# Performance work log

Measured on AMD Instinct MI355X. Metric: run time of the kernel, lower is better.

Reference implementation:

```python
import jax, jax.numpy as jnp
import numpy as np

N, C, H, W = 8, 80, 100, 152          # batch, fg classes, stride-8 feature map of 800x1216 image
STRIDE = 8
P = H * W                              # points in this level
PRE_NMS_THRESH = 0.05                  # cfg.post.INFERENCE_TH
PRE_NMS_TOP_N = 1000                   # cfg.post.PRE_NMS_TOP_N
NMS_THRESH = 0.6                       # cfg.post.NMS_TH
POST_NMS_TOP_N = 100                   # cfg.post.DETECTIONS_PER_IMG
MIN_SIZE = 0.0
CLASS_OFFSET = 1.0e5                   # per-class NMS via coordinate-offset trick


def setup_inputs():
    key = jax.random.key(0)
    k1, k2, k3 = jax.random.split(key, 3)
    ys, xs = jnp.meshgrid(jnp.arange(H), jnp.arange(W), indexing='ij')
    locations = (jnp.stack([xs.reshape(-1), ys.reshape(-1)], axis=1).astype(jnp.float32) * STRIDE + STRIDE // 2)
    box_cls = jax.random.normal(k1, (N, C, H, W), jnp.float32) - 2.0
    box_regression = jax.random.uniform(k2, (N, 4, H, W), jnp.float32) * 64.0
    centerness = jax.random.normal(k3, (N, 1, H, W), jnp.float32)
    im_info = jnp.tile(jnp.array([[H * STRIDE, W * STRIDE]], jnp.float32), (N, 1))
    return {'locations': locations, 'box_cls': box_cls, 'box_regression': box_regression,
            'centerness': centerness, 'im_info': im_info}


def _iou_matrix(boxes):
    # boxes: [K, 4] (x1, y1, x2, y2)
    area = jnp.clip(boxes[:, 2] - boxes[:, 0], 0) * jnp.clip(boxes[:, 3] - boxes[:, 1], 0)
    lt = jnp.maximum(boxes[:, None, :2], boxes[None, :, :2])
    rb = jnp.minimum(boxes[:, None, 2:], boxes[None, :, 2:])
    wh = jnp.clip(rb - lt, 0)
    inter = wh[..., 0] * wh[..., 1]
    return inter / (area[:, None] + area[None, :] - inter + 1e-9)


def _single_image(locations, cls_logits, reg, ctr_logits, info):
    # [C,H,W] -> [P,C] matches permute(0,2,3,1).reshape(-1,C)
    cls = jax.nn.sigmoid(cls_logits.reshape(C, P).T)
    ctr = jax.nn.sigmoid(ctr_logits.reshape(P))
    cand = cls > PRE_NMS_THRESH
    scores = cls * ctr[:, None]
    flat = jnp.where(cand, scores, 0.0).reshape(-1)          # [P*C], zeros = non-candidates
    topv, topi = jax.lax.top_k(flat, PRE_NMS_TOP_N)          # pre-NMS top-n (sorted desc)
    loc = topi // C
    label = topi % C + 1
    valid = topv > 0.0
    r = reg.reshape(4, P).T[loc]                             # [K, 4] (l, t, r, b)
    pt = locations[loc]                                      # [K, 2]
    h_im, w_im = info[0], info[1]
    x1 = jnp.clip(pt[:, 0] - r[:, 0], 0.0, w_im - 1.0)
    y1 = jnp.clip(pt[:, 1] - r[:, 1], 0.0, h_im - 1.0)
    x2 = jnp.clip(pt[:, 0] + r[:, 2], 0.0, w_im - 1.0)
    y2 = jnp.clip(pt[:, 1] + r[:, 3], 0.0, h_im - 1.0)
    boxes = jnp.stack([x1, y1, x2, y2], axis=1)
    valid = valid & (x2 - x1 >= MIN_SIZE) & (y2 - y1 >= MIN_SIZE)  # remove_small_boxes
    sc = jnp.where(valid, topv, 0.0)
    # offset boxes by class so cross-class IoU is 0 -> equivalent to per-class NMS
    ob = boxes + (label.astype(boxes.dtype) * CLASS_OFFSET)[:, None]
    iou = _iou_matrix(ob)
    idx = jnp.arange(PRE_NMS_TOP_N)
    def body(i, keep):
        alive = keep[i] & valid[i]
        sup = alive & (iou[i] > NMS_THRESH) & (idx > i)
        return keep & ~sup
    keep = jax.lax.fori_loop(0, PRE_NMS_TOP_N, body, valid)  # greedy NMS (score-sorted)
    final_sc = jnp.where(keep, sc, 0.0)
    fv, fi = jax.lax.top_k(final_sc, POST_NMS_TOP_N)         # detections-per-image cap
    out = jnp.concatenate([boxes[fi], label[fi][:, None].astype(boxes.dtype), fv[:, None]], axis=1)
    return jnp.where((fv > 0.0)[:, None], out, 0.0)          # [POST_NMS_TOP_N, 6]


def reference(locations, box_cls, box_regression, centerness, im_info):
    # -> [N, POST_NMS_TOP_N, 6] = (x1, y1, x2, y2, label, score), zero-padded rows invalid
    return jax.vmap(lambda c, r, t, i: _single_image(locations, c, r, t, i))(
        box_cls, box_regression, centerness, im_info)
```

## Files before the change

### kernel.cpp

```cpp
#include <hip/hip_runtime.h>
#include <stdint.h>

#define NIMG 8
#define NCLS 80
#define HF 100
#define WF 152
#define NPTS (HF*WF)
#define NPC (NPTS*NCLS)
#define NF4 (NPC/4)
#define TOPK 1000
#define NSH 8
#define SHCAP 512
#define SORTN 4096
#define LBUF 1024
#define POSTK 100
#define HBLK 297
#define RBLK (SORTN/256)
#define SCHUNK 32
#define SSTRIDE 9500
#define SM_T 65

static constexpr size_t B_CNT  = 0;
static constexpr size_t B_META = B_CNT + (size_t)NIMG*NSH*4;
static constexpr size_t B_SKEY = (B_META + NIMG*4*4 + 7) & ~(size_t)7;
static constexpr size_t B_CTRS = (B_SKEY + (size_t)NIMG*1024*8 + 15) & ~(size_t)15;
static constexpr size_t B_CAND = (B_CTRS + (size_t)NIMG*NPTS*4 + 15) & ~(size_t)15;
static constexpr size_t B_BOX  = B_CAND + (size_t)NIMG*NSH*SHCAP*8;
static constexpr size_t B_OBOX = B_BOX + (size_t)NIMG*TOPK*16;
static constexpr size_t B_SC   = B_OBOX + (size_t)NIMG*TOPK*16;
static constexpr size_t B_VAL  = B_SC + (size_t)NIMG*TOPK*4;
static constexpr size_t B_LAB  = B_VAL + (size_t)NIMG*TOPK*4;
static constexpr size_t B_KEEP = B_LAB + (size_t)NIMG*TOPK*4;
#define ZWORDS (NIMG*NSH + NIMG*4)

__device__ __forceinline__ float sigm(float x){ return 1.0f / (1.0f + expf(-x)); }

__global__ void __launch_bounds__(256)
k_ctrsig(const float* __restrict__ ctr, float* __restrict__ ctr_sig,
         uint32_t* __restrict__ zr, uint64_t* __restrict__ skey){
  const int gid = blockIdx.x * 256 + threadIdx.x;
  const int nthr = 119 * 256;
  if (gid < NIMG*NPTS/4){
    float4 v = ((const float4*)ctr)[gid];
    float4 o;
    o.x = sigm(v.x); o.y = sigm(v.y); o.z = sigm(v.z); o.w = sigm(v.w);
    ((float4*)ctr_sig)[gid] = o;
  }
  for (int i = gid; i < ZWORDS; i += nthr) zr[i] = 0u;
  for (int i = gid; i < NIMG*1024; i += nthr) skey[i] = 0ull;
}

__global__ void __launch_bounds__(256)
k_sample(const float* __restrict__ box_cls, const float* __restrict__ ctr_sig,
         uint32_t* __restrict__ meta){
  __shared__ uint32_t h[4096];
  __shared__ uint32_t psum[256], suff[256];
  const int n = blockIdx.x;
  const int t = threadIdx.x;
  for (int i = t; i < 4096; i += 256) h[i] = 0;
  __syncthreads();
  const float4* cls4 = (const float4*)(box_cls + (size_t)n * NPC);
  const float* cs = ctr_sig + (size_t)n * NPTS;
  for (int c0 = 0; c0 < SCHUNK; c0 += 4){
    float4 a[4], b[4];
    #pragma unroll
    for (int k = 0; k < 4; ++k){
      int g = (c0 + k) * SSTRIDE + t;
      a[k] = cls4[g];
      uint32_t p0 = ((uint32_t)(g << 2)) % (uint32_t)NPTS;
      b[k] = *(const float4*)(cs + p0);
    }
    __builtin_amdgcn_sched_barrier(0);
    #pragma unroll
    for (int k = 0; k < 4; ++k){
      float sv[4] = {a[k].x, a[k].y, a[k].z, a[k].w};
      float cv[4] = {b[k].x, b[k].y, b[k].z, b[k].w};
      #pragma unroll
      for (int j = 0; j < 4; ++j){
        float s = sigm(sv[j]);
        if (s > 0.05f){
          float sc = s * cv[j];
          if (sc > 0.0f) atomicAdd(&h[__float_as_uint(sc) >> 18], 1u);
        }
      }
    }
  }
  __syncthreads();
  uint32_t s = 0;
  #pragma unroll
  for (int i = 0; i < 16; ++i) s += h[t * 16 + i];
  psum[t] = s;
  __syncthreads();
  if (t == 0){
    uint32_t acc = 0;
    for (int seg = 255; seg >= 0; --seg){ suff[seg] = acc; acc += psum[seg]; }
  }
  __syncthreads();
  if (suff[t] < SM_T && suff[t] + psum[t] >= SM_T){
    uint32_t acc = suff[t];
    for (int b = t * 16 + 15; b >= t * 16; --b){
      uint32_t hb = h[b];
      if (acc + hb >= SM_T){
        meta[n * 4 + 1] = ((uint32_t)b) << 18;
        break;
      }
      acc += hb;
    }
  }
}

__global__ void __launch_bounds__(256)
k_main(const float* __restrict__ box_cls, const float* __restrict__ ctr_sig,
       const uint32_t* __restrict__ meta,
       uint32_t* __restrict__ cnt, uint64_t* __restrict__ cand){
  __shared__ uint64_t buf[LBUF];
  __shared__ uint32_t lcnt;
  __shared__ uint32_t gbase;
  const int n = blockIdx.y;
  const uint32_t Traw = meta[n * 4 + 1];
  if (threadIdx.x == 0) lcnt = 0;
  __syncthreads();
  const float4* cls4 = (const float4*)(box_cls + (size_t)n * NPC);
  const float* cs = ctr_sig + (size_t)n * NPTS;
  const int base4 = blockIdx.x * 1024 + threadIdx.x;
  float4 a[4], b[4];
  int p0a[4], ca[4];
  bool ok[4];
  #pragma unroll
  for (int k = 0; k < 4; ++k){
    int i4 = base4 + k * 256;
    ok[k] = (i4 < NF4);
    if (ok[k]){
      a[k] = cls4[i4];
      uint32_t e0 = (uint32_t)(i4 << 2);
      uint32_t c = e0 / (uint32_t)NPTS;
      uint32_t p0 = e0 - c * (uint32_t)NPTS;
      ca[k] = (int)c; p0a[k] = (int)p0;
      b[k] = *(const float4*)(cs + p0);
    }
  }
  __builtin_amdgcn_sched_barrier(0);
  #pragma unroll
  for (int k = 0; k < 4; ++k){
    if (!ok[k]) continue;
    float sv[4] = {a[k].x, a[k].y, a[k].z, a[k].w};
    float cv[4] = {b[k].x, b[k].y, b[k].z, b[k].w};
    #pragma unroll
    for (int j = 0; j < 4; ++j){
      float s = sigm(sv[j]);
      if (s > 0.05f){
        float sc = s * cv[j];
        if (sc > 0.0f){
          uint32_t bits = __float_as_uint(sc);
          if (bits >= Traw){
            uint32_t f = (uint32_t)(p0a[k] + j) * NCLS + (uint32_t)ca[k];
            uint32_t pos = atomicAdd(&lcnt, 1u);
            if (pos < LBUF)
              buf[pos] = ((uint64_t)bits << 32) | (uint64_t)(0xFFFFFFFFu - f);
          }
        }
      }
    }
  }
  __syncthreads();
  uint32_t c = lcnt; if (c > LBUF) c = LBUF;
  const int sh = blockIdx.x & (NSH - 1);
  if (threadIdx.x == 0 && c) gbase = atomicAdd(&cnt[n * NSH + sh], c);
  __syncthreads();
  for (uint32_t i = threadIdx.x; i < c; i += 256){
    uint32_t p = gbase + i;
    if (p < SHCAP) cand[(((size_t)n * NSH + sh) << 9) + p] = buf[i];
  }
}

__global__ void __launch_bounds__(1024)
k_fallback(const float* __restrict__ box_cls, const float* __restrict__ ctr_sig,
           const uint32_t* __restrict__ meta,
           uint32_t* __restrict__ cnt, uint64_t* __restrict__ cand){
  __shared__ uint32_t h[4096];
  __shared__ uint32_t psum[256], suff[256];
  __shared__ uint32_t ok_s, T14_s, ctr_s;
  const int n = blockIdx.x;
  const int t = threadIdx.x;
  if (t == 0){
    uint32_t total = 0, bad = 0;
    for (int s = 0; s < NSH; ++s){
      uint32_t c = cnt[n * NSH + s];
      total += c; bad |= (c > SHCAP) ? 1u : 0u;
    }
    uint32_t Traw = meta[n * 4 + 1];
    ok_s = (!bad && (total >= TOPK || Traw == 0u)) ? 1u : 0u;
    T14_s = 0; ctr_s = 0;
  }
  __syncthreads();
  if (ok_s) return;
  for (int i = t; i < 4096; i += 1024) h[i] = 0;
  __syncthreads();
  const float* cls = box_cls + (size_t)n * NPC;
  const float* cs = ctr_sig + (size_t)n * NPTS;
  for (int e = t; e < NPC; e += 1024){
    int c = e / NPTS, p = e - c * NPTS;
    float s = sigm(cls[e]);
    if (s > 0.05f){
      float sc = s * cs[p];
      if (sc > 0.0f) atomicAdd(&h[__float_as_uint(sc) >> 18], 1u);
    }
  }
  __syncthreads();
  if (t < 256){
    uint32_t s = 0;
    #pragma unroll
    for (int i = 0; i < 16; ++i) s += h[t * 16 + i];
    psum[t] = s;
  }
  __syncthreads();
  if (t == 0){
    uint32_t acc = 0;
    for (int seg = 255; seg >= 0; --seg){ suff[seg] = acc; acc += psum[seg]; }
  }
  __syncthreads();
  if (t < 256 && suff[t] < TOPK && suff[t] + psum[t] >= TOPK){
    uint32_t acc = suff[t];
    for (int b = t * 16 + 15; b >= t * 16; --b){
      uint32_t hb = h[b];
      if (acc + hb >= TOPK){ T14_s = (uint32_t)b; break; }
      acc += hb;
    }
  }
  __syncthreads();
  const uint32_t Traw2 = T14_s << 18;
  if (t < NSH) cnt[n * NSH + t] = 0;
  __syncthreads();
  for (int e = t; e < NPC; e += 1024){
    int c = e / NPTS, p = e - c * NPTS;
    float s = sigm(cls[e]);
    if (s > 0.05f){
      float sc = s * cs[p];
      if (sc > 0.0f){
        uint32_t bits = __float_as_uint(sc);
        if (bits >= Traw2){
          uint32_t f = (uint32_t)p * NCLS + (uint32_t)c;
          uint32_t pos = atomicAdd(&ctr_s, 1u);
          if (pos < SORTN)
            cand[((size_t)n * NSH << 9) + pos] = ((uint64_t)bits << 32) | (uint64_t)(0xFFFFFFFFu - f);
        }
      }
    }
  }
  __syncthreads();
  if (t < NSH){
    uint32_t total = ctr_s; if (total > SORTN) total = SORTN;
    int lo = t * SHCAP;
    cnt[n * NSH + t] = ((int)total > lo) ? ((total - lo > SHCAP) ? SHCAP : total - lo) : 0u;
  }
}

__global__ void __launch_bounds__(256)
k_rank(const uint32_t* __restrict__ cnt, const uint64_t* __restrict__ cand,
       uint64_t* __restrict__ skey){
  __shared__ alignas(16) uint64_t keys[SORTN + 64];
  __shared__ uint32_t cs_s[NSH], pre_s[NSH + 1];
  const int n = blockIdx.y;
  const int t = threadIdx.x;
  const int lane = t & 63;
  if (t == 0){
    uint32_t acc = 0;
    for (int s = 0; s < NSH; ++s){
      uint32_t c = cnt[n * NSH + s]; if (c > SHCAP) c = SHCAP;
      cs_s[s] = c; pre_s[s] = acc; acc += c;
    }
    pre_s[NSH] = acc;
  }
  __syncthreads();
  const int total = (int)pre_s[NSH];
  const int base = blockIdx.x * 256;
  if (base >= total) return;
  for (int i = t; i < SORTN; i += 256){
    int s = i >> 9, j = i & (SHCAP - 1);
    if ((uint32_t)j < cs_s[s])
      keys[pre_s[s] + j] = cand[(((size_t)n * NSH + s) << 9) + j];
  }
  if (t < 64) keys[total + t] = 0ull;
  __syncthreads();
  const int g = base + t;
  const uint64_t my = (g < total) ? keys[g] : 0ull;
  uint32_t rank = 0;
  const int tot64 = (total + 63) & ~63;
  for (int i = 0; i < tot64; i += 64){
    uint64_t kv = keys[i + lane];
    uint32_t kvlo = (uint32_t)kv, kvhi = (uint32_t)(kv >> 32);
    #pragma unroll
    for (int s = 0; s < 64; ++s){
      uint32_t ohi = (uint32_t)__builtin_amdgcn_readlane((int)kvhi, s);
      uint32_t olo = (uint32_t)__builtin_amdgcn_readlane((int)kvlo, s);
      uint64_t other = ((uint64_t)ohi << 32) | (uint64_t)olo;
      rank += (other > my) ? 1u : 0u;
    }
  }
  if (g < total && rank < TOPK)
    skey[(size_t)n * 1024 + rank] = my;
}

__global__ void __launch_bounds__(1024)
k_decode(const uint64_t* __restrict__ skey,
         const float* __restrict__ locations, const float* __restrict__ box_reg,
         const float* __restrict__ im_info,
         float* __restrict__ boxw, float* __restrict__ oboxw, float* __restrict__ scw,
         uint32_t* __restrict__ valw, uint32_t* __restrict__ labw){
  const int n = blockIdx.x;
  const int t = threadIdx.x;
  if (t < TOPK){
    uint64_t kk = skey[(size_t)n * 1024 + t];
    uint32_t bits = (uint32_t)(kk >> 32);
    uint32_t fi = 0xFFFFFFFFu - (uint32_t)(kk & 0xFFFFFFFFull);
    float v = __uint_as_float(bits);
    int loc = 0, ci = 0;
    if (v > 0.0f){ loc = (int)(fi / NCLS); ci = (int)(fi - (uint32_t)loc * NCLS); }
    float px = locations[2 * loc], py = locations[2 * loc + 1];
    const float* rg = box_reg + (size_t)n * 4 * NPTS;
    float rl = rg[loc], rt = rg[NPTS + loc], rr = rg[2 * NPTS + loc], rb = rg[3 * NPTS + loc];
    float h_im = im_info[n * 2 + 0], w_im = im_info[n * 2 + 1];
    float x1 = fminf(fmaxf(px - rl, 0.0f), w_im - 1.0f);
    float y1 = fminf(fmaxf(py - rt, 0.0f), h_im - 1.0f);
    float x2 = fminf(fmaxf(px + rr, 0.0f), w_im - 1.0f);
    float y2 = fminf(fmaxf(py + rb, 0.0f), h_im - 1.0f);
    bool valid = (v > 0.0f) && (__fsub_rn(x2, x1) >= 0.0f) && (__fsub_rn(y2, y1) >= 0.0f);
    float scv = valid ? v : 0.0f;
    float lab = (float)(ci + 1);
    float off = __fmul_rn(lab, 100000.0f);
    size_t b4 = ((size_t)n * TOPK + t) * 4;
    boxw[b4 + 0] = x1; boxw[b4 + 1] = y1; boxw[b4 + 2] = x2; boxw[b4 + 3] = y2;
    oboxw[b4 + 0] = __fadd_rn(x1, off); oboxw[b4 + 1] = __fadd_rn(y1, off);
    oboxw[b4 + 2] = __fadd_rn(x2, off); oboxw[b4 + 3] = __fadd_rn(y2, off);
    size_t b1 = (size_t)n * TOPK + t;
    scw[b1] = scv; valw[b1] = valid ? 1u : 0u; labw[b1] = (uint32_t)(ci + 1);
  }
}

__global__ void __launch_bounds__(64)
k_nms(const uint32_t* __restrict__ labw, const float* __restrict__ oboxw,
      const uint32_t* __restrict__ valw, uint32_t* __restrict__ keepw){
  const int n = blockIdx.y;
  const int c = blockIdx.x;
  const int L = threadIdx.x;
  __shared__ uint16_t lst_s[TOPK];
  const uint32_t target = (uint32_t)(c + 1);
  uint32_t kcnt = 0;
  for (int i0 = 0; i0 < TOPK; i0 += 64){
    int slot = i0 + L;
    uint32_t lab = (slot < TOPK) ? labw[n * TOPK + slot] : 0u;
    bool m = (lab == target);
    uint64_t mask = __ballot(m);
    uint32_t pre = (uint32_t)__popcll(mask & ((1ull << L) - 1ull));
    if (m) lst_s[kcnt + pre] = (uint16_t)slot;
    kcnt += (uint32_t)__popcll(mask);
  }
  __syncthreads();
  if (kcnt == 0) return;
  if (kcnt <= 64){
    int gi = 0, kp = 0;
    float b0 = 0, b1 = 0, b2 = 0, b3 = 0, ar = 0;
    if (L < (int)kcnt){
      gi = (int)lst_s[L];
      size_t a4 = ((size_t)n * TOPK + gi) * 4;
      b0 = oboxw[a4 + 0]; b1 = oboxw[a4 + 1]; b2 = oboxw[a4 + 2]; b3 = oboxw[a4 + 3];
      kp = (valw[n * TOPK + gi] != 0) ? 1 : 0;
      ar = __fmul_rn(fmaxf(__fsub_rn(b2, b0), 0.0f), fmaxf(__fsub_rn(b3, b1), 0.0f));
    }
    for (int i = 0; i + 1 < (int)kcnt; ++i){
      int alive = __shfl(kp, i);
      float xi0 = __shfl(b0, i), xi1 = __shfl(b1, i), xi2 = __shfl(b2, i), xi3 = __shfl(b3, i);
      float ai = __shfl(ar, i);
      if (alive && L > i && kp){
        float ltx = fmaxf(xi0, b0), lty = fmaxf(xi1, b1);
        float rbx = fminf(xi2, b2), rby = fminf(xi3, b3);
        float w = fmaxf(__fsub_rn(rbx, ltx), 0.0f);
        float h = fmaxf(__fsub_rn(rby, lty), 0.0f);
        float inter = __fmul_rn(w, h);
        float den = __fadd_rn(__fsub_rn(__fadd_rn(ai, ar), inter), 1e-9f);
        if (inter / den > 0.6f) kp = 0;
      }
    }
    if (L < (int)kcnt) keepw[n * TOPK + gi] = (uint32_t)kp;
  } else if (L == 0){
    for (uint32_t i = 0; i < kcnt; ++i){
      int gi = (int)lst_s[i];
      keepw[n * TOPK + gi] = valw[n * TOPK + gi];
    }
    for (uint32_t i = 0; i < kcnt; ++i){
      int gi = (int)lst_s[i];
      if (!keepw[n * TOPK + gi]) continue;
      size_t a4 = ((size_t)n * TOPK + gi) * 4;
      float x0 = oboxw[a4], x1 = oboxw[a4 + 1], x2 = oboxw[a4 + 2], x3 = oboxw[a4 + 3];
      float ai = __fmul_rn(fmaxf(__fsub_rn(x2, x0), 0.0f), fmaxf(__fsub_rn(x3, x1), 0.0f));
      for (uint32_t j = i + 1; j < kcnt; ++j){
        int gj = (int)lst_s[j];
        if (!keepw[n * TOPK + gj]) continue;
        size_t c4 = ((size_t)n * TOPK + gj) * 4;
        float y0 = oboxw[c4], y1 = oboxw[c4 + 1], y2 = oboxw[c4 + 2], y3 = oboxw[c4 + 3];
        float aj = __fmul_rn(fmaxf(__fsub_rn(y2, y0), 0.0f), fmaxf(__fsub_rn(y3, y1), 0.0f));
        float ltx = fmaxf(x0, y0), lty = fmaxf(x1, y1);
        float rbx = fminf(x2, y2), rby = fminf(x3, y3);
        float w = fmaxf(__fsub_rn(rbx, ltx), 0.0f);
        float h = fmaxf(__fsub_rn(rby, lty), 0.0f);
        float inter = __fmul_rn(w, h);
        float den = __fadd_rn(__fsub_rn(__fadd_rn(ai, aj), inter), 1e-9f);
        if (inter / den > 0.6f) keepw[n * TOPK + gj] = 0;
      }
    }
  }
}

__global__ void __launch_bounds__(256)
k_final(const uint32_t* __restrict__ keepw, const float* __restrict__ boxw,
        const uint32_t* __restrict__ labw, const float* __restrict__ scw,
        float* __restrict__ out){
  const int n = blockIdx.x;
  __shared__ uint16_t fi_s[TOPK];
  __shared__ uint32_t wsum[4];
  const int t = threadIdx.x;
  const int i0 = t * 4;
  uint32_t f[4];
  #pragma unroll
  for (int j = 0; j < 4; ++j)
    f[j] = (i0 + j < TOPK) ? keepw[n * TOPK + i0 + j] : 0u;
  uint32_t lsum = f[0] + f[1] + f[2] + f[3];
  uint32_t sc = lsum;
  #pragma unroll
  for (int d = 1; d < 64; d <<= 1){
    uint32_t v = __shfl_up(sc, d);
    if ((t & 63) >= d) sc += v;
  }
  if ((t & 63) == 63) wsum[t >> 6] = sc;
  __syncthreads();
  uint32_t base = sc - lsum;
  for (int w = 0; w < (t >> 6); ++w) base += wsum[w];
  uint32_t p = base;
  #pragma unroll
  for (int j = 0; j < 4; ++j){
    if (f[j]){ if (p < TOPK) fi_s[p] = (uint16_t)(i0 + j); ++p; }
  }
  __syncthreads();
  uint32_t total = wsum[0] + wsum[1] + wsum[2] + wsum[3];
  if (t < POSTK){
    float* row = out + ((size_t)n * POSTK + t) * 6;
    if (t < (int)total){
      int i = (int)fi_s[t];
      size_t b4 = ((size_t)n * TOPK + i) * 4;
      row[0] = boxw[b4]; row[1] = boxw[b4 + 1]; row[2] = boxw[b4 + 2]; row[3] = boxw[b4 + 3];
      row[4] = (float)labw[n * TOPK + i]; row[5] = scw[n * TOPK + i];
    } else {
      row[0] = 0.0f; row[1] = 0.0f; row[2] = 0.0f;
      row[3] = 0.0f; row[4] = 0.0f; row[5] = 0.0f;
    }
  }
}

extern "C" void kernel_launch(void* const* d_in, const int* in_sizes, int n_in,
                              void* d_out, int out_size, void* d_ws, size_t ws_size,
                              hipStream_t stream){
  const float* locations = (const float*)d_in[0];
  const float* box_cls   = (const float*)d_in[1];
  const float* box_reg   = (const float*)d_in[2];
  const float* ctr       = (const float*)d_in[3];
  const float* im_info   = (const float*)d_in[4];
  float* out = (float*)d_out;
  char* ws = (char*)d_ws;
  uint32_t* cnt  = (uint32_t*)(ws + B_CNT);
  uint32_t* meta = (uint32_t*)(ws + B_META);
  uint64_t* skey = (uint64_t*)(ws + B_SKEY);
  float*    ctrs = (float*)(ws + B_CTRS);
  uint64_t* cand = (uint64_t*)(ws + B_CAND);
  float*    boxw  = (float*)(ws + B_BOX);
  float*    oboxw = (float*)(ws + B_OBOX);
  float*    scw   = (float*)(ws + B_SC);
  uint32_t* valw  = (uint32_t*)(ws + B_VAL);
  uint32_t* labw  = (uint32_t*)(ws + B_LAB);
  uint32_t* keepw = (uint32_t*)(ws + B_KEEP);

  k_ctrsig<<<dim3(119), 256, 0, stream>>>(ctr, ctrs, cnt, skey);
  k_sample<<<dim3(NIMG), 256, 0, stream>>>(box_cls, ctrs, meta);
  k_main<<<dim3(HBLK, NIMG), 256, 0, stream>>>(box_cls, ctrs, meta, cnt, cand);
  k_fallback<<<dim3(NIMG), 1024, 0, stream>>>(box_cls, ctrs, meta, cnt, cand);
  k_rank<<<dim3(RBLK, NIMG), 256, 0, stream>>>(cnt, cand, skey);
  k_decode<<<NIMG, 1024, 0, stream>>>(skey, locations, box_reg, im_info,
                                      boxw, oboxw, scw, valw, labw);
  k_nms<<<dim3(NCLS, NIMG), 64, 0, stream>>>(labw, oboxw, valw, keepw);
  k_final<<<NIMG, 256, 0, stream>>>(keepw, boxw, labw, scw, out);
}
```

Baseline: 185.1 us.

## Merge prep kernels and fuse NMS with final gather via last-block counter

Merges the centerness-sigmoid/zeroing kernel and the threshold-sampling kernel into one launch. The sampling blocks now compute the centerness sigmoid inline from raw input instead of reading the precomputed buffer. NMS and the final compaction are fused: each per-class block bumps a per-image done counter, and the last block compacts the keep flags and writes the output rows. This removes two launches and their gaps, at the cost of atomics, fences and redundant sigmoid work in the sampler.

```diff
diff --git a/kernel.cpp b/kernel.cpp
--- a/kernel.cpp
+++ b/kernel.cpp
@@ -19,9 +19,11 @@
 #define SCHUNK 32
 #define SSTRIDE 9500
 #define SM_T 65
+#define PBLK 127
 
 static constexpr size_t B_CNT  = 0;
-static constexpr size_t B_META = B_CNT + (size_t)NIMG*NSH*4;
+static constexpr size_t B_DONE = B_CNT + (size_t)NIMG*NSH*4;
+static constexpr size_t B_META = B_DONE + NIMG*4;
 static constexpr size_t B_SKEY = (B_META + NIMG*4*4 + 7) & ~(size_t)7;
 static constexpr size_t B_CTRS = (B_SKEY + (size_t)NIMG*1024*8 + 15) & ~(size_t)15;
 static constexpr size_t B_CAND = (B_CTRS + (size_t)NIMG*NPTS*4 + 15) & ~(size_t)15;
@@ -31,50 +33,51 @@
 static constexpr size_t B_VAL  = B_SC + (size_t)NIMG*TOPK*4;
 static constexpr size_t B_LAB  = B_VAL + (size_t)NIMG*TOPK*4;
 static constexpr size_t B_KEEP = B_LAB + (size_t)NIMG*TOPK*4;
-#define ZWORDS (NIMG*NSH + NIMG*4)
+#define ZWORDS (NIMG*NSH + NIMG)
 
 __device__ __forceinline__ float sigm(float x){ return 1.0f / (1.0f + expf(-x)); }
 
 __global__ void __launch_bounds__(256)
-k_ctrsig(const float* __restrict__ ctr, float* __restrict__ ctr_sig,
-         uint32_t* __restrict__ zr, uint64_t* __restrict__ skey){
-  const int gid = blockIdx.x * 256 + threadIdx.x;
-  const int nthr = 119 * 256;
-  if (gid < NIMG*NPTS/4){
-    float4 v = ((const float4*)ctr)[gid];
-    float4 o;
-    o.x = sigm(v.x); o.y = sigm(v.y); o.z = sigm(v.z); o.w = sigm(v.w);
-    ((float4*)ctr_sig)[gid] = o;
-  }
-  for (int i = gid; i < ZWORDS; i += nthr) zr[i] = 0u;
-  for (int i = gid; i < NIMG*1024; i += nthr) skey[i] = 0ull;
-}
-
-__global__ void __launch_bounds__(256)
-k_sample(const float* __restrict__ box_cls, const float* __restrict__ ctr_sig,
-         uint32_t* __restrict__ meta){
+k_prep(const float* __restrict__ ctr, const float* __restrict__ box_cls,
+       float* __restrict__ ctr_sig, uint32_t* __restrict__ zr,
+       uint64_t* __restrict__ skey, uint32_t* __restrict__ meta){
+  const int b = blockIdx.x;
+  const int t = threadIdx.x;
+  if (b < 119){
+    const int gid = b * 256 + t;
+    const int nthr = 119 * 256;
+    if (gid < NIMG*NPTS/4){
+      float4 v = ((const float4*)ctr)[gid];
+      float4 o;
+      o.x = sigm(v.x); o.y = sigm(v.y); o.z = sigm(v.z); o.w = sigm(v.w);
+      ((float4*)ctr_sig)[gid] = o;
+    }
+    for (int i = gid; i < ZWORDS; i += nthr) zr[i] = 0u;
+    for (int i = gid; i < NIMG*1024; i += nthr) skey[i] = 0ull;
+    return;
+  }
+  const int n = b - 119;
   __shared__ uint32_t h[4096];
   __shared__ uint32_t psum[256], suff[256];
-  const int n = blockIdx.x;
-  const int t = threadIdx.x;
   for (int i = t; i < 4096; i += 256) h[i] = 0;
+  if (t == 0) meta[n * 4 + 1] = 0u;
   __syncthreads();
   const float4* cls4 = (const float4*)(box_cls + (size_t)n * NPC);
-  const float* cs = ctr_sig + (size_t)n * NPTS;
+  const float* ctq = ctr + (size_t)n * NPTS;
   for (int c0 = 0; c0 < SCHUNK; c0 += 4){
-    float4 a[4], b[4];
+    float4 a[4], rb[4];
     #pragma unroll
     for (int k = 0; k < 4; ++k){
       int g = (c0 + k) * SSTRIDE + t;
       a[k] = cls4[g];
       uint32_t p0 = ((uint32_t)(g << 2)) % (uint32_t)NPTS;
-      b[k] = *(const float4*)(cs + p0);
+      rb[k] = *(const float4*)(ctq + p0);
     }
     __builtin_amdgcn_sched_barrier(0);
     #pragma unroll
     for (int k = 0; k < 4; ++k){
       float sv[4] = {a[k].x, a[k].y, a[k].z, a[k].w};
-      float cv[4] = {b[k].x, b[k].y, b[k].z, b[k].w};
+      float cv[4] = {sigm(rb[k].x), sigm(rb[k].y), sigm(rb[k].z), sigm(rb[k].w)};
       #pragma unroll
       for (int j = 0; j < 4; ++j){
         float s = sigm(sv[j]);
@@ -98,10 +101,10 @@
   __syncthreads();
   if (suff[t] < SM_T && suff[t] + psum[t] >= SM_T){
     uint32_t acc = suff[t];
-    for (int b = t * 16 + 15; b >= t * 16; --b){
-      uint32_t hb = h[b];
+    for (int bb = t * 16 + 15; bb >= t * 16; --bb){
+      uint32_t hb = h[bb];
       if (acc + hb >= SM_T){
-        meta[n * 4 + 1] = ((uint32_t)b) << 18;
+        meta[n * 4 + 1] = ((uint32_t)bb) << 18;
         break;
       }
       acc += hb;
@@ -338,8 +341,11 @@
 }
 
 __global__ void __launch_bounds__(64)
-k_nms(const uint32_t* __restrict__ labw, const float* __restrict__ oboxw,
-      const uint32_t* __restrict__ valw, uint32_t* __restrict__ keepw){
+k_nmsfinal(const uint32_t* __restrict__ labw, const float* __restrict__ oboxw,
+           const uint32_t* __restrict__ valw, const float* __restrict__ boxw,
+           const float* __restrict__ scw,
+           uint32_t* __restrict__ keepw, uint32_t* __restrict__ done,
+           float* __restrict__ out){
   const int n = blockIdx.y;
   const int c = blockIdx.x;
   const int L = threadIdx.x;
@@ -356,102 +362,91 @@
     kcnt += (uint32_t)__popcll(mask);
   }
   __syncthreads();
-  if (kcnt == 0) return;
-  if (kcnt <= 64){
-    int gi = 0, kp = 0;
-    float b0 = 0, b1 = 0, b2 = 0, b3 = 0, ar = 0;
-    if (L < (int)kcnt){
-      gi = (int)lst_s[L];
-      size_t a4 = ((size_t)n * TOPK + gi) * 4;
-      b0 = oboxw[a4 + 0]; b1 = oboxw[a4 + 1]; b2 = oboxw[a4 + 2]; b3 = oboxw[a4 + 3];
-      kp = (valw[n * TOPK + gi] != 0) ? 1 : 0;
-      ar = __fmul_rn(fmaxf(__fsub_rn(b2, b0), 0.0f), fmaxf(__fsub_rn(b3, b1), 0.0f));
-    }
-    for (int i = 0; i + 1 < (int)kcnt; ++i){
-      int alive = __shfl(kp, i);
-      float xi0 = __shfl(b0, i), xi1 = __shfl(b1, i), xi2 = __shfl(b2, i), xi3 = __shfl(b3, i);
-      float ai = __shfl(ar, i);
-      if (alive && L > i && kp){
-        float ltx = fmaxf(xi0, b0), lty = fmaxf(xi1, b1);
-        float rbx = fminf(xi2, b2), rby = fminf(xi3, b3);
-        float w = fmaxf(__fsub_rn(rbx, ltx), 0.0f);
-        float h = fmaxf(__fsub_rn(rby, lty), 0.0f);
-        float inter = __fmul_rn(w, h);
-        float den = __fadd_rn(__fsub_rn(__fadd_rn(ai, ar), inter), 1e-9f);
-        if (inter / den > 0.6f) kp = 0;
-      }
-    }
-    if (L < (int)kcnt) keepw[n * TOPK + gi] = (uint32_t)kp;
-  } else if (L == 0){
-    for (uint32_t i = 0; i < kcnt; ++i){
-      int gi = (int)lst_s[i];
-      keepw[n * TOPK + gi] = valw[n * TOPK + gi];
-    }
-    for (uint32_t i = 0; i < kcnt; ++i){
-      int gi = (int)lst_s[i];
-      if (!keepw[n * TOPK + gi]) continue;
-      size_t a4 = ((size_t)n * TOPK + gi) * 4;
-      float x0 = oboxw[a4], x1 = oboxw[a4 + 1], x2 = oboxw[a4 + 2], x3 = oboxw[a4 + 3];
-      float ai = __fmul_rn(fmaxf(__fsub_rn(x2, x0), 0.0f), fmaxf(__fsub_rn(x3, x1), 0.0f));
-      for (uint32_t j = i + 1; j < kcnt; ++j){
-        int gj = (int)lst_s[j];
-        if (!keepw[n * TOPK + gj]) continue;
-        size_t c4 = ((size_t)n * TOPK + gj) * 4;
-        float y0 = oboxw[c4], y1 = oboxw[c4 + 1], y2 = oboxw[c4 + 2], y3 = oboxw[c4 + 3];
-        float aj = __fmul_rn(fmaxf(__fsub_rn(y2, y0), 0.0f), fmaxf(__fsub_rn(y3, y1), 0.0f));
-        float ltx = fmaxf(x0, y0), lty = fmaxf(x1, y1);
-        float rbx = fminf(x2, y2), rby = fminf(x3, y3);
-        float w = fmaxf(__fsub_rn(rbx, ltx), 0.0f);
-        float h = fmaxf(__fsub_rn(rby, lty), 0.0f);
-        float inter = __fmul_rn(w, h);
-        float den = __fadd_rn(__fsub_rn(__fadd_rn(ai, aj), inter), 1e-9f);
-        if (inter / den > 0.6f) keepw[n * TOPK + gj] = 0;
-      }
-    }
-  }
-}
-
-__global__ void __launch_bounds__(256)
-k_final(const uint32_t* __restrict__ keepw, const float* __restrict__ boxw,
-        const uint32_t* __restrict__ labw, const float* __restrict__ scw,
-        float* __restrict__ out){
-  const int n = blockIdx.x;
-  __shared__ uint16_t fi_s[TOPK];
-  __shared__ uint32_t wsum[4];
-  const int t = threadIdx.x;
-  const int i0 = t * 4;
-  uint32_t f[4];
-  #pragma unroll
-  for (int j = 0; j < 4; ++j)
-    f[j] = (i0 + j < TOPK) ? keepw[n * TOPK + i0 + j] : 0u;
-  uint32_t lsum = f[0] + f[1] + f[2] + f[3];
-  uint32_t sc = lsum;
-  #pragma unroll
-  for (int d = 1; d < 64; d <<= 1){
-    uint32_t v = __shfl_up(sc, d);
-    if ((t & 63) >= d) sc += v;
-  }
-  if ((t & 63) == 63) wsum[t >> 6] = sc;
-  __syncthreads();
-  uint32_t base = sc - lsum;
-  for (int w = 0; w < (t >> 6); ++w) base += wsum[w];
-  uint32_t p = base;
-  #pragma unroll
-  for (int j = 0; j < 4; ++j){
-    if (f[j]){ if (p < TOPK) fi_s[p] = (uint16_t)(i0 + j); ++p; }
-  }
-  __syncthreads();
-  uint32_t total = wsum[0] + wsum[1] + wsum[2] + wsum[3];
-  if (t < POSTK){
-    float* row = out + ((size_t)n * POSTK + t) * 6;
-    if (t < (int)total){
-      int i = (int)fi_s[t];
-      size_t b4 = ((size_t)n * TOPK + i) * 4;
-      row[0] = boxw[b4]; row[1] = boxw[b4 + 1]; row[2] = boxw[b4 + 2]; row[3] = boxw[b4 + 3];
-      row[4] = (float)labw[n * TOPK + i]; row[5] = scw[n * TOPK + i];
-    } else {
-      row[0] = 0.0f; row[1] = 0.0f; row[2] = 0.0f;
-      row[3] = 0.0f; row[4] = 0.0f; row[5] = 0.0f;
+  if (kcnt != 0){
+    if (kcnt <= 64){
+      int gi = 0, kp = 0;
+      float b0 = 0, b1 = 0, b2 = 0, b3 = 0, ar = 0;
+      if (L < (int)kcnt){
+        gi = (int)lst_s[L];
+        size_t a4 = ((size_t)n * TOPK + gi) * 4;
+        b0 = oboxw[a4 + 0]; b1 = oboxw[a4 + 1]; b2 = oboxw[a4 + 2]; b3 = oboxw[a4 + 3];
+        kp = (valw[n * TOPK + gi] != 0) ? 1 : 0;
+        ar = __fmul_rn(fmaxf(__fsub_rn(b2, b0), 0.0f), fmaxf(__fsub_rn(b3, b1), 0.0f));
+      }
+      for (int i = 0; i + 1 < (int)kcnt; ++i){
+        int alive = __shfl(kp, i);
+        float xi0 = __shfl(b0, i), xi1 = __shfl(b1, i), xi2 = __shfl(b2, i), xi3 = __shfl(b3, i);
+        float ai = __shfl(ar, i);
+        if (alive && L > i && kp){
+          float ltx = fmaxf(xi0, b0), lty = fmaxf(xi1, b1);
+          float rbx = fminf(xi2, b2), rby = fminf(xi3, b3);
+          float w = fmaxf(__fsub_rn(rbx, ltx), 0.0f);
+          float h = fmaxf(__fsub_rn(rby, lty), 0.0f);
+          float inter = __fmul_rn(w, h);
+          float den = __fadd_rn(__fsub_rn(__fadd_rn(ai, ar), inter), 1e-9f);
+          if (inter / den > 0.6f) kp = 0;
+        }
+      }
+      if (L < (int)kcnt) keepw[n * TOPK + gi] = (uint32_t)kp;
+    } else if (L == 0){
+      for (uint32_t i = 0; i < kcnt; ++i){
+        int gi = (int)lst_s[i];
+        keepw[n * TOPK + gi] = valw[n * TOPK + gi];
+      }
+      for (uint32_t i = 0; i < kcnt; ++i){
+        int gi = (int)lst_s[i];
+        if (!keepw[n * TOPK + gi]) continue;
+        size_t a4 = ((size_t)n * TOPK + gi) * 4;
+        float x0 = oboxw[a4], x1 = oboxw[a4 + 1], x2 = oboxw[a4 + 2], x3 = oboxw[a4 + 3];
+        float ai = __fmul_rn(fmaxf(__fsub_rn(x2, x0), 0.0f), fmaxf(__fsub_rn(x3, x1), 0.0f));
+        for (uint32_t j = i + 1; j < kcnt; ++j){
+          int gj = (int)lst_s[j];
+          if (!keepw[n * TOPK + gj]) continue;
+          size_t c4 = ((size_t)n * TOPK + gj) * 4;
+          float y0 = oboxw[c4], y1 = oboxw[c4 + 1], y2 = oboxw[c4 + 2], y3 = oboxw[c4 + 3];
+          float aj = __fmul_rn(fmaxf(__fsub_rn(y2, y0), 0.0f), fmaxf(__fsub_rn(y3, y1), 0.0f));
+          float ltx = fmaxf(x0, y0), lty = fmaxf(x1, y1);
+          float rbx = fminf(x2, y2), rby = fminf(x3, y3);
+          float w = fmaxf(__fsub_rn(rbx, ltx), 0.0f);
+          float h = fmaxf(__fsub_rn(rby, lty), 0.0f);
+          float inter = __fmul_rn(w, h);
+          float den = __fadd_rn(__fsub_rn(__fadd_rn(ai, aj), inter), 1e-9f);
+          if (inter / den > 0.6f) keepw[n * TOPK + gj] = 0;
+        }
+      }
+    }
+  }
+  __syncthreads();
+  __threadfence();
+  uint32_t tk = 0;
+  if (L == 0) tk = (uint32_t)atomicAdd(&done[n], 1u);
+  tk = (uint32_t)__shfl((int)tk, 0);
+  if (tk == NCLS - 1){
+    __threadfence();
+    __shared__ uint16_t fi[POSTK];
+    uint32_t cc = 0;
+    for (int i0 = 0; i0 < TOPK; i0 += 64){
+      int slot = i0 + L;
+      uint32_t kp = (slot < TOPK) ? keepw[n * TOPK + slot] : 0u;
+      uint64_t mask = __ballot(kp != 0u);
+      uint32_t pre = (uint32_t)__popcll(mask & ((1ull << L) - 1ull));
+      uint32_t p = cc + pre;
+      if (kp && p < POSTK) fi[p] = (uint16_t)slot;
+      cc += (uint32_t)__popcll(mask);
+      if (cc >= POSTK) break;
+    }
+    __syncthreads();
+    for (int r = L; r < POSTK; r += 64){
+      float* row = out + ((size_t)n * POSTK + r) * 6;
+      if (r < (int)cc){
+        int i = (int)fi[r];
+        size_t b4 = ((size_t)n * TOPK + i) * 4;
+        row[0] = boxw[b4]; row[1] = boxw[b4 + 1]; row[2] = boxw[b4 + 2]; row[3] = boxw[b4 + 3];
+        row[4] = (float)labw[n * TOPK + i]; row[5] = scw[n * TOPK + i];
+      } else {
+        row[0] = 0.0f; row[1] = 0.0f; row[2] = 0.0f;
+        row[3] = 0.0f; row[4] = 0.0f; row[5] = 0.0f;
+      }
     }
   }
 }
@@ -467,6 +462,7 @@
   float* out = (float*)d_out;
   char* ws = (char*)d_ws;
   uint32_t* cnt  = (uint32_t*)(ws + B_CNT);
+  uint32_t* done = (uint32_t*)(ws + B_DONE);
   uint32_t* meta = (uint32_t*)(ws + B_META);
   uint64_t* skey = (uint64_t*)(ws + B_SKEY);
   float*    ctrs = (float*)(ws + B_CTRS);
@@ -478,13 +474,12 @@
   uint32_t* labw  = (uint32_t*)(ws + B_LAB);
   uint32_t* keepw = (uint32_t*)(ws + B_KEEP);
 
-  k_ctrsig<<<dim3(119), 256, 0, stream>>>(ctr, ctrs, cnt, skey);
-  k_sample<<<dim3(NIMG), 256, 0, stream>>>(box_cls, ctrs, meta);
+  k_prep<<<dim3(PBLK), 256, 0, stream>>>(ctr, box_cls, ctrs, cnt, skey, meta);
   k_main<<<dim3(HBLK, NIMG), 256, 0, stream>>>(box_cls, ctrs, meta, cnt, cand);
   k_fallback<<<dim3(NIMG), 1024, 0, stream>>>(box_cls, ctrs, meta, cnt, cand);
   k_rank<<<dim3(RBLK, NIMG), 256, 0, stream>>>(cnt, cand, skey);
   k_decode<<<NIMG, 1024, 0, stream>>>(skey, locations, box_reg, im_info,
                                       boxw, oboxw, scw, valw, labw);
-  k_nms<<<dim3(NCLS, NIMG), 64, 0, stream>>>(labw, oboxw, valw, keepw);
-  k_final<<<NIMG, 256, 0, stream>>>(keepw, boxw, labw, scw, out);
-}
+  k_nmsfinal<<<dim3(NCLS, NIMG), 64, 0, stream>>>(labw, oboxw, valw, boxw, scw,
+                                                  keepw, done, out);
+}
```

Result: slower. 196.8 us (+6.3%).
